# Kernel optimization log

Hardware: AMD Instinct MI355X
Metric: run time of the kernel (lower is better)

The kernel has to match this reference:

```python
import jax, jax.numpy as jnp
import numpy as np

N = 20000      # nodes
E = 320000     # edges (avg degree 16)
D = 256        # embedding_dim
H = 8          # num_heads
DH = D // H    # head_dim = 32
ED = 64        # edge_dim
FF = 4 * D     # feed-forward hidden
EPS = 1e-5


def setup_inputs() -> dict:
    key = jax.random.key(0)
    ks = jax.random.split(key, 32)

    def lin_w(k, i, o):
        return (jax.random.normal(k, (i, o), jnp.float32) / np.sqrt(i)).astype(jnp.float32)

    return {
        "x": jax.random.normal(ks[0], (N, D), jnp.float32),
        "edge_features": jax.random.normal(ks[1], (E, ED), jnp.float32),
        "edge_weights": jax.random.uniform(ks[2], (E,), jnp.float32),
        "edge_index": jax.random.randint(ks[3], (2, E), 0, N, dtype=jnp.int32),
        "Wq": lin_w(ks[4], D, D), "bq": jnp.zeros((D,), jnp.float32),
        "Wk": lin_w(ks[5], D, D), "bk": jnp.zeros((D,), jnp.float32),
        "Wv": lin_w(ks[6], D, D), "bv": jnp.zeros((D,), jnp.float32),
        "We": lin_w(ks[7], ED, DH), "be": jnp.zeros((DH,), jnp.float32),
        "Wo": lin_w(ks[8], D, D), "bo": jnp.zeros((D,), jnp.float32),
        "ln1_g": jnp.ones((D,), jnp.float32), "ln1_b": jnp.zeros((D,), jnp.float32),
        "ln2_g": jnp.ones((D,), jnp.float32), "ln2_b": jnp.zeros((D,), jnp.float32),
        "W1": lin_w(ks[9], D, FF), "b1": jnp.zeros((FF,), jnp.float32),
        "W2": lin_w(ks[10], FF, D), "b2": jnp.zeros((D,), jnp.float32),
        "alpha": jnp.ones((1,), jnp.float32),
        "beta": jnp.ones((1,), jnp.float32),
    }


def _layernorm(x, g, b):
    m = jnp.mean(x, axis=-1, keepdims=True)
    v = jnp.var(x, axis=-1, keepdims=True)
    return (x - m) * jax.lax.rsqrt(v + EPS) * g + b


def _edge_attention(xn, edge_index, ef, ew, Wq, bq, Wk, bk, Wv, bv, We, be, Wo, bo):
    n = xn.shape[0]
    scale = DH ** -0.5
    q = (xn @ Wq + bq).reshape(n, H, DH)
    k = (xn @ Wk + bk).reshape(n, H, DH)
    v = (xn @ Wv + bv).reshape(n, H, DH)
    src, dst = edge_index[0], edge_index[1]
    ep = ef @ We + be                               # [E, DH], shared across heads
    # per-edge, per-head scores: q[dst] . (k[src] + edge_proj)
    scores = jnp.einsum('ehd,ehd->eh', q[dst], k[src] + ep[:, None, :]) * scale
    scores = scores * ew[:, None]
    # segment softmax over incoming edges of each dst node
    m = jax.ops.segment_max(scores, dst, num_segments=n)
    m = jnp.where(jnp.isfinite(m), m, 0.0)          # nodes with no incoming edges
    ex = jnp.exp(scores - m[dst])
    s = jax.ops.segment_sum(ex, dst, num_segments=n)
    attn = ex / s[dst]                              # [E, H]
    # scatter-weighted V aggregation; nodes with no edges stay zero (matches torch)
    out = jax.ops.segment_sum(attn[:, :, None] * v[src], dst, num_segments=n)
    out = out.reshape(n, D) @ Wo + bo
    return out


def reference(x, edge_features, edge_weights, edge_index,
              Wq, bq, Wk, bk, Wv, bv, We, be, Wo, bo,
              ln1_g, ln1_b, ln2_g, ln2_b, W1, b1, W2, b2, alpha, beta):
    xn = _layernorm(x, ln1_g, ln1_b)
    attn_out = _edge_attention(xn, edge_index, edge_features, edge_weights,
                               Wq, bq, Wk, bk, Wv, bv, We, be, Wo, bo)
    x = x + alpha * attn_out
    xn = _layernorm(x, ln2_g, ln2_b)
    ff = jax.nn.gelu(xn @ W1 + b1, approximate=False) @ W2 + b2
    x = x + beta * ff
    return x
```

## Files before the change

kernel.cpp:

```cpp
#include <hip/hip_runtime.h>
#include <math.h>

#define NN 20000
#define EE 320000
#define DD 256
#define HH 8
#define DHD 32
#define EDF 64
#define FFD 1024

typedef unsigned short u16;
typedef __attribute__((ext_vector_type(8))) __bf16 bf16x8;
typedef __attribute__((ext_vector_type(8))) unsigned short u16x8;
typedef __attribute__((ext_vector_type(4))) float f32x4;

#define XN_OFF   (0)
#define AGGB_OFF (2560000)
#define X1_OFF   (5120000)
#define QKV_OFF  (10240000)
#define EP_OFF   (25600000)
#define WT_OFF   (35840000)
#define BQKV_OFF (36240000)
#define CSR_OFF  (36250000)

__device__ __forceinline__ u16 f2bf(float f) {
    unsigned u = __float_as_uint(f);
    return (u16)((u + 0x7FFFu + ((u >> 16) & 1u)) >> 16);
}
__device__ __forceinline__ float bf2f(u16 h) {
    return __uint_as_float(((unsigned)h) << 16);
}
__device__ __forceinline__ float gelu_exact(float v) {
    return 0.5f * v * (1.0f + erff(v * 0.70710678118654752f));
}
__device__ __forceinline__ int xcd_swz(int bid, int nwg) {
    int q = nwg >> 3, r = nwg & 7;
    int xcd = bid & 7, i = bid >> 3;
    return (xcd < r ? xcd * (q + 1) : r * (q + 1) + (xcd - r) * q) + i;
}

#define GLDS16(g, l) __builtin_amdgcn_global_load_lds(             \
    (__attribute__((address_space(1))) void*)(g),                  \
    (__attribute__((address_space(3))) void*)(l), 16, 0, 0)

__device__ __forceinline__ void ln_body(const float* __restrict__ x,
                                        const float* __restrict__ g,
                                        const float* __restrict__ b,
                                        u16* __restrict__ out, int vb) {
    int row = vb * 4 + (threadIdx.x >> 6);
    if (row >= NN) return;
    int lane = threadIdx.x & 63;
    float4 v = *(const float4*)&x[(size_t)row * DD + lane * 4];
    float s  = v.x + v.y + v.z + v.w;
    float ss = v.x * v.x + v.y * v.y + v.z * v.z + v.w * v.w;
    #pragma unroll
    for (int o = 32; o >= 1; o >>= 1) {
        s  += __shfl_xor(s, o);
        ss += __shfl_xor(ss, o);
    }
    float mean = s * (1.0f / DD);
    float var  = ss * (1.0f / DD) - mean * mean;
    float inv  = rsqrtf(var + 1e-5f);
    float4 gg = *(const float4*)&g[lane * 4];
    float4 bb = *(const float4*)&b[lane * 4];
    ushort4 o4;
    o4.x = f2bf((v.x - mean) * inv * gg.x + bb.x);
    o4.y = f2bf((v.y - mean) * inv * gg.y + bb.y);
    o4.z = f2bf((v.z - mean) * inv * gg.z + bb.z);
    o4.w = f2bf((v.w - mean) * inv * gg.w + bb.w);
    *(ushort4*)&out[(size_t)row * DD + lane * 4] = o4;
}

__global__ __launch_bounds__(256) void ln_kernel(const float* __restrict__ x,
                                                 const float* __restrict__ g,
                                                 const float* __restrict__ b,
                                                 u16* __restrict__ out) {
    ln_body(x, g, b, out, blockIdx.x);
}

__device__ __forceinline__ void transp_body(const float* __restrict__ src,
                                            u16* __restrict__ dst,
                                            int K, int N, int k0, int n0) {
    __shared__ float Ws[64][65];
    int t = threadIdx.x;
    int rr = t >> 4, cc = (t & 15) * 4;
    if (n0 + cc < N) {
        #pragma unroll
        for (int p = 0; p < 4; p++) {
            int k = rr + p * 16;
            float4 v = *(const float4*)&src[(size_t)(k0 + k) * N + n0 + cc];
            Ws[k][cc + 0] = v.x; Ws[k][cc + 1] = v.y;
            Ws[k][cc + 2] = v.z; Ws[k][cc + 3] = v.w;
        }
    }
    __syncthreads();
    int n = t >> 2, kc = (t & 3) * 16;
    if (n0 + n < N) {
        u16 o[16];
        #pragma unroll
        for (int j = 0; j < 16; j++) o[j] = f2bf(Ws[kc + j][n]);
        u16* dp = dst + (size_t)(n0 + n) * K + k0 + kc;
        *(ushort4*)(dp + 0)  = *(ushort4*)&o[0];
        *(ushort4*)(dp + 4)  = *(ushort4*)&o[4];
        *(ushort4*)(dp + 8)  = *(ushort4*)&o[8];
        *(ushort4*)(dp + 12) = *(ushort4*)&o[12];
    }
}

__global__ __launch_bounds__(256) void prep_count_ln_kernel(
    const float* __restrict__ Wq, const float* __restrict__ Wk,
    const float* __restrict__ Wv, const float* __restrict__ Wo,
    const float* __restrict__ W1, const float* __restrict__ W2,
    const float* __restrict__ We,
    const float* __restrict__ bq, const float* __restrict__ bk,
    const float* __restrict__ bv,
    u16* __restrict__ WqkvT, u16* __restrict__ WoT, u16* __restrict__ W1T,
    u16* __restrict__ W2T, u16* __restrict__ WeT, float* __restrict__ bqkv,
    const int* __restrict__ ei, int* __restrict__ counts,
    const float* __restrict__ x, const float* __restrict__ ln1g,
    const float* __restrict__ ln1b, u16* __restrict__ xn) {
    int b = blockIdx.x;
    if (b < 193) {
        const float* src; u16* dst; int K, N, ti;
        if      (b < 16)  { src = Wq; dst = WqkvT;          K = 256;  N = 256;  ti = b; }
        else if (b < 32)  { src = Wk; dst = WqkvT + 65536;  K = 256;  N = 256;  ti = b - 16; }
        else if (b < 48)  { src = Wv; dst = WqkvT + 131072; K = 256;  N = 256;  ti = b - 32; }
        else if (b < 64)  { src = Wo; dst = WoT;            K = 256;  N = 256;  ti = b - 48; }
        else if (b < 128) { src = W1; dst = W1T;            K = 256;  N = 1024; ti = b - 64; }
        else if (b < 192) { src = W2; dst = W2T;            K = 1024; N = 256;  ti = b - 128; }
        else              { src = We; dst = WeT;            K = 64;   N = 32;   ti = 0; }
        int ntn = N >> 6; if (ntn == 0) ntn = 1;
        int tk = ti / ntn, tn = ti % ntn;
        transp_body(src, dst, K, N, tk * 64, tn * 64);
    } else if (b == 193) {
        int t = threadIdx.x;
        bqkv[t] = bq[t];
        bqkv[256 + t] = bk[t];
        bqkv[512 + t] = bv[t];
    } else if (b < 1444) {
        int e = (b - 194) * 256 + threadIdx.x;
        if (e < EE) atomicAdd(&counts[ei[EE + e]], 1);
    } else {
        ln_body(x, ln1g, ln1b, xn, b - 1444);
    }
}

template <int BM, int BN, int EPI>
__device__ __forceinline__ void gemm_body(
    char* smem,
    const u16* __restrict__ A, const u16* __restrict__ BT,
    const float* __restrict__ bias,
    float* __restrict__ Cf, u16* __restrict__ Cb,
    const float* __restrict__ res, const float* __restrict__ scale,
    int M, int K, int N, int bxx, int byy)
{
    constexpr int FM = BM / 32, FN = BN / 32;
    constexpr int nA = BM / 32, nB = BN / 32;
    constexpr int NST = (nA > nB) ? nA : nB;
    u16* Asm = (u16*)smem;
    u16* Bsm = (u16*)(smem + BM * 64 * 2);
    const int tid  = threadIdx.x;
    const int lane = tid & 63;
    const int w    = tid >> 6;
    const int wr   = w >> 1, wc = w & 1;
    const int bm   = bxx * BM;
    const int bn   = byy * BN;

    f32x4 acc[FM][FN] = {};

    int st_row[NST], st_src[NST], st_dst[NST];
    #pragma unroll
    for (int i = 0; i < NST; i++) {
        int base  = i * 4096 + w * 1024;
        int off   = base + lane * 16;
        int row   = off >> 7;
        int inner = off & 127;
        st_row[i] = row;
        st_src[i] = (inner ^ ((row & 7) << 4)) >> 1;
        st_dst[i] = base;
    }
    const int arow0 = wr * (BM / 2) + (lane & 15);
    const int brow0 = wc * (BN / 2) + (lane & 15);
    const int kb0   = (lane >> 4) * 16;

    for (int k0 = 0; k0 < K; k0 += 64) {
        #pragma unroll
        for (int i = 0; i < nA; i++) {
            int r = bm + st_row[i]; if (r > M - 1) r = M - 1;
            GLDS16(A + (size_t)r * K + k0 + st_src[i], (char*)Asm + st_dst[i]);
        }
        #pragma unroll
        for (int i = 0; i < nB; i++) {
            int r = bn + st_row[i];
            GLDS16(BT + (size_t)r * K + k0 + st_src[i], (char*)Bsm + st_dst[i]);
        }
        asm volatile("s_waitcnt vmcnt(0)" ::: "memory");
        __syncthreads();
        #pragma unroll
        for (int s = 0; s < 2; s++) {
            bf16x8 af[FM], bfv[FN];
            #pragma unroll
            for (int i = 0; i < FM; i++) {
                int row  = arow0 + i * 16;
                int byte = (row << 7) + ((kb0 + s * 64) ^ ((row & 7) << 4));
                af[i] = *(const bf16x8*)((const char*)Asm + byte);
            }
            #pragma unroll
            for (int j = 0; j < FN; j++) {
                int row  = brow0 + j * 16;
                int byte = (row << 7) + ((kb0 + s * 64) ^ ((row & 7) << 4));
                bfv[j] = *(const bf16x8*)((const char*)Bsm + byte);
            }
            #pragma unroll
            for (int i = 0; i < FM; i++)
                #pragma unroll
                for (int j = 0; j < FN; j++)
                    acc[i][j] = __builtin_amdgcn_mfma_f32_16x16x32_bf16(
                        af[i], bfv[j], acc[i][j], 0, 0, 0);
        }
        __syncthreads();
    }

    float sc = 0.f;
    if constexpr (EPI == 2) sc = scale[0];
    const int col0 = bn + wc * (BN / 2) + (lane & 15);
    const int row0 = bm + wr * (BM / 2) + ((lane >> 4) << 2);
    #pragma unroll
    for (int i = 0; i < FM; i++) {
        #pragma unroll
        for (int j = 0; j < FN; j++) {
            int col = col0 + j * 16;
            float bb = bias[col];
            #pragma unroll
            for (int r = 0; r < 4; r++) {
                int row = row0 + i * 16 + r;
                if (row < M) {
                    float o = acc[i][j][r] + bb;
                    if constexpr (EPI == 1) {
                        Cb[(size_t)row * N + col] = f2bf(gelu_exact(o));
                    } else if constexpr (EPI == 2) {
                        Cf[(size_t)row * N + col] = res[(size_t)row * N + col] + sc * o;
                    } else if constexpr (EPI == 3) {
                        if (col < 256) {
                            Cb[(size_t)row * 256 + col] = f2bf(o * 0.17677669529663689f);
                        } else if (col < 512) {
                            Cb[(size_t)NN * 256 + (size_t)row * 512 + (col - 256)] = f2bf(o);
                        } else {
                            Cb[(size_t)NN * 256 + (size_t)row * 512 + 256 + (col - 512)] = f2bf(o);
                        }
                    } else {
                        Cf[(size_t)row * N + col] = o;
                    }
                }
            }
        }
    }
}

template <int BM, int BN, int EPI>
__global__ __launch_bounds__(256) void gemm_bf16(
    const u16* __restrict__ A, const u16* __restrict__ BT,
    const float* __restrict__ bias,
    float* __restrict__ Cf, u16* __restrict__ Cb,
    const float* __restrict__ res, const float* __restrict__ scale,
    int M, int K, int N, int nwg, int nby) {
    __shared__ char smem[(BM + BN) * 64 * 2];
    int wk = xcd_swz(blockIdx.x, nwg);
    gemm_body<BM, BN, EPI>(smem, A, BT, bias, Cf, Cb, res, scale, M, K, N,
                           wk / nby, wk % nby);
}

__device__ __forceinline__ void ep_body(char* smem,
                                        const float* __restrict__ ef,
                                        const u16* __restrict__ WeT,
                                        const float* __restrict__ be,
                                        const int* __restrict__ epos,
                                        u16* __restrict__ epc, int blk) {
    const int tid  = threadIdx.x;
    const int lane = tid & 63;
    const int w    = tid >> 6;
    const int e0b  = blk * 128;

    #pragma unroll
    for (int j = 0; j < 8; j++) {
        int gidx = (w * 8 + j) * 64 + lane;
        int e    = gidx >> 4;
        int cs   = (gidx & 15) << 4;
        int c    = cs ^ ((e & 15) << 4);
        GLDS16((const char*)ef + (size_t)(e0b + e) * 256 + c,
               smem + (w * 8 + j) * 1024);
    }
    asm volatile("s_waitcnt vmcnt(0)" ::: "memory");
    __syncthreads();

    const int ar = lane & 15;
    f32x4 acc[2][2] = {};
    #pragma unroll
    for (int t = 0; t < 2; t++) {
        int r = w * 32 + t * 16 + ar;
        const char* base = smem + r * 256;
        #pragma unroll
        for (int s = 0; s < 2; s++) {
            int cbyte = (lane >> 4) * 32 + s * 128;
            float4 a0 = *(const float4*)(base + ((cbyte)      ^ (ar << 4)));
            float4 a1 = *(const float4*)(base + ((cbyte + 16) ^ (ar << 4)));
            bf16x8 af;
            af[0] = (__bf16)a0.x; af[1] = (__bf16)a0.y; af[2] = (__bf16)a0.z; af[3] = (__bf16)a0.w;
            af[4] = (__bf16)a1.x; af[5] = (__bf16)a1.y; af[6] = (__bf16)a1.z; af[7] = (__bf16)a1.w;
            #pragma unroll
            for (int j = 0; j < 2; j++) {
                bf16x8 bf = *(const bf16x8*)&WeT[(size_t)(j * 16 + ar) * EDF + s * 32 + ((lane >> 4) * 8)];
                acc[t][j] = __builtin_amdgcn_mfma_f32_16x16x32_bf16(af, bf, acc[t][j], 0, 0, 0);
            }
        }
    }
    __syncthreads();
    u16* outl = (u16*)smem;
    int* posl = (int*)(smem + 8192);
    if (tid < 128) posl[tid] = epos[e0b + tid];
    const int row0 = (lane >> 4) << 2;
    #pragma unroll
    for (int t = 0; t < 2; t++)
        #pragma unroll
        for (int j = 0; j < 2; j++)
            #pragma unroll
            for (int rr = 0; rr < 4; rr++) {
                int row = w * 32 + t * 16 + row0 + rr;
                int col = j * 16 + ar;
                outl[row * 32 + col] = f2bf(acc[t][j][rr] + be[col]);
            }
    __syncthreads();
    #pragma unroll
    for (int c2 = 0; c2 < 2; c2++) {
        int ch = tid + c2 * 256;
        int row = ch >> 2, part = ch & 3;
        u16x8 v = *(const u16x8*)&outl[row * 32 + part * 8];
        *(u16x8*)&epc[(size_t)posl[row] * DHD + part * 8] = v;
    }
}

__global__ __launch_bounds__(256) void qkv_ep_kernel(
    const u16* __restrict__ xn, const u16* __restrict__ WqkvT,
    const float* __restrict__ bqkv, u16* __restrict__ qb,
    const float* __restrict__ ef, const u16* __restrict__ WeT,
    const float* __restrict__ be, const int* __restrict__ epos,
    u16* __restrict__ epc) {
    __shared__ char smem[32768];
    int b = blockIdx.x;
    if (b < 942) {
        int wk = xcd_swz(b, 942);
        gemm_body<128, 128, 3>(smem, xn, WqkvT, bqkv, nullptr, qb, nullptr,
                               nullptr, NN, DD, 768, wk / 6, wk % 6);
    } else {
        ep_body(smem, ef, WeT, be, epos, epc, b - 942);
    }
}

__global__ __launch_bounds__(1024) void scan_kernel(const int* __restrict__ counts,
                                                    int* __restrict__ row_start,
                                                    int* __restrict__ cursor,
                                                    int* __restrict__ dcursor) {
    __shared__ int part[1024];
    __shared__ int hist[64][16];
    const int CH = 20;
    int t = threadIdx.x;
    if (t < 64) {
        #pragma unroll
        for (int s = 0; s < 16; s++) hist[t][s] = 0;
    }
    __syncthreads();
    int base = t * CH;
    int sub = t & 15;
    int loc[CH];
    int s = 0;
    #pragma unroll
    for (int i = 0; i < CH; i++) {
        int idx = base + i;
        int c = (idx < NN) ? counts[idx] : 0;
        if (idx < NN) atomicAdd(&hist[min(c, 63)][sub], 1);
        loc[i] = s;
        s += c;
    }
    part[t] = s;
    __syncthreads();
    for (int o = 1; o < 1024; o <<= 1) {
        int vv = (t >= o) ? part[t - o] : 0;
        __syncthreads();
        part[t] += vv;
        __syncthreads();
    }
    int off = (t > 0) ? part[t - 1] : 0;
    #pragma unroll
    for (int i = 0; i < CH; i++) {
        int idx = base + i;
        if (idx < NN) {
            int rs = off + loc[i];
            row_start[idx] = rs;
            cursor[idx] = rs;
        }
    }
    if (t == 1023) row_start[NN] = part[1023];
    if (t < 64) {
        int st = 0;
        for (int b = 63; b > t; --b) {
            #pragma unroll
            for (int sj = 0; sj < 16; sj++) st += hist[b][sj];
        }
        dcursor[t] = st;
    }
}

__global__ __launch_bounds__(256) void fill_kernel(const int* __restrict__ ei,
                                                   const float* __restrict__ ew,
                                                   int* __restrict__ cursor,
                                                   int2* __restrict__ csr,
                                                   int* __restrict__ epos,
                                                   const int* __restrict__ counts,
                                                   int* __restrict__ dcursor,
                                                   int* __restrict__ order) {
    int b = blockIdx.x;
    if (b < EE / 256) {
        int e = b * 256 + threadIdx.x;
        int src = ei[e];
        int dst = ei[EE + e];
        int pos = atomicAdd(&cursor[dst], 1);
        csr[pos] = make_int2(src, __float_as_int(ew[e] * 1.44269504088896f));
        epos[e] = pos;
    } else {
        __shared__ int lhist[64];
        __shared__ int lbase[64];
        int t = threadIdx.x;
        if (t < 64) lhist[t] = 0;
        __syncthreads();
        int n = (b - EE / 256) * 256 + t;
        int d = -1, lpos = 0;
        if (n < NN) {
            d = min(counts[n], 63);
            lpos = atomicAdd(&lhist[d], 1);
        }
        __syncthreads();
        if (t < 64 && lhist[t] > 0) lbase[t] = atomicAdd(&dcursor[t], lhist[t]);
        __syncthreads();
        if (n < NN) order[lbase[d] + lpos] = n;
    }
}

__global__ __launch_bounds__(256) void attn_kernel(const u16* __restrict__ qb,
                                                   const u16* __restrict__ kv,
                                                   const u16* __restrict__ epc,
                                                   const int2* __restrict__ csr,
                                                   const int* __restrict__ row_start,
                                                   const int* __restrict__ order,
                                                   u16* __restrict__ aggb) {
    const int dst  = order[blockIdx.x * 4 + (threadIdx.x >> 6)];
    const int lane = threadIdx.x & 63;
    const int g    = lane & 7;
    const int d0   = (lane >> 3) * 32 + g * 4;
    const int beg = row_start[dst];
    const int end = row_start[dst + 1];
    ushort4 q4 = *(const ushort4*)&qb[(size_t)dst * DD + d0];
    float4 qv = make_float4(bf2f(q4.x), bf2f(q4.y), bf2f(q4.z), bf2f(q4.w));
    float ss = 0.f;
    float4 acc = make_float4(0.f, 0.f, 0.f, 0.f);

    int i = beg;
    if ((i & 1) && i < end) {
        int2 p = csr[i];
        ushort4 ka = *(const ushort4*)&kv[(size_t)p.x * 512 + d0];
        ushort4 va = *(const ushort4*)&kv[(size_t)p.x * 512 + 256 + d0];
        ushort4 e4 = *(const ushort4*)&epc[(size_t)i * DHD + g * 4];
        float k0 = bf2f(ka.x) + bf2f(e4.x);
        float k1 = bf2f(ka.y) + bf2f(e4.y);
        float k2 = bf2f(ka.z) + bf2f(e4.z);
        float k3 = bf2f(ka.w) + bf2f(e4.w);
        float pv = fmaf(qv.x, k0, fmaf(qv.y, k1, fmaf(qv.z, k2, qv.w * k3)));
        #pragma unroll
        for (int o = 4; o >= 1; o >>= 1) pv += __shfl_xor(pv, o);
        float wq = exp2f(pv * __int_as_float(p.y));
        ss += wq;
        acc.x = fmaf(wq, bf2f(va.x), acc.x);
        acc.y = fmaf(wq, bf2f(va.y), acc.y);
        acc.z = fmaf(wq, bf2f(va.z), acc.z);
        acc.w = fmaf(wq, bf2f(va.w), acc.w);
        ++i;
    }
    for (; i + 4 <= end; i += 4) {
        int4 c01 = *(const int4*)&csr[i];
        int4 c23 = *(const int4*)&csr[i + 2];
        int   sr[4] = {c01.x, c01.z, c23.x, c23.z};
        float wt[4] = {__int_as_float(c01.y), __int_as_float(c01.w),
                       __int_as_float(c23.y), __int_as_float(c23.w)};
        ushort4 ka[4], va[4], e4[4];
        #pragma unroll
        for (int u = 0; u < 4; u++) {
            ka[u] = *(const ushort4*)&kv[(size_t)sr[u] * 512 + d0];
            va[u] = *(const ushort4*)&kv[(size_t)sr[u] * 512 + 256 + d0];
            e4[u] = *(const ushort4*)&epc[(size_t)(i + u) * DHD + g * 4];
        }
        float pp[4];
        #pragma unroll
        for (int u = 0; u < 4; u++) {
            float k0 = bf2f(ka[u].x) + bf2f(e4[u].x);
            float k1 = bf2f(ka[u].y) + bf2f(e4[u].y);
            float k2 = bf2f(ka[u].z) + bf2f(e4[u].z);
            float k3 = bf2f(ka[u].w) + bf2f(e4[u].w);
            pp[u] = fmaf(qv.x, k0, fmaf(qv.y, k1, fmaf(qv.z, k2, qv.w * k3)));
        }
        #pragma unroll
        for (int o = 4; o >= 1; o >>= 1) {
            #pragma unroll
            for (int u = 0; u < 4; u++) pp[u] += __shfl_xor(pp[u], o);
        }
        #pragma unroll
        for (int u = 0; u < 4; u++) {
            float wq = exp2f(pp[u] * wt[u]);
            ss += wq;
            acc.x = fmaf(wq, bf2f(va[u].x), acc.x);
            acc.y = fmaf(wq, bf2f(va[u].y), acc.y);
            acc.z = fmaf(wq, bf2f(va[u].z), acc.z);
            acc.w = fmaf(wq, bf2f(va[u].w), acc.w);
        }
    }
    for (; i < end; ++i) {
        int2 p = csr[i];
        ushort4 ka = *(const ushort4*)&kv[(size_t)p.x * 512 + d0];
        ushort4 va = *(const ushort4*)&kv[(size_t)p.x * 512 + 256 + d0];
        ushort4 e4 = *(const ushort4*)&epc[(size_t)i * DHD + g * 4];
        float k0 = bf2f(ka.x) + bf2f(e4.x);
        float k1 = bf2f(ka.y) + bf2f(e4.y);
        float k2 = bf2f(ka.z) + bf2f(e4.z);
        float k3 = bf2f(ka.w) + bf2f(e4.w);
        float pv = fmaf(qv.x, k0, fmaf(qv.y, k1, fmaf(qv.z, k2, qv.w * k3)));
        #pragma unroll
        for (int o = 4; o >= 1; o >>= 1) pv += __shfl_xor(pv, o);
        float wq = exp2f(pv * __int_as_float(p.y));
        ss += wq;
        acc.x = fmaf(wq, bf2f(va.x), acc.x);
        acc.y = fmaf(wq, bf2f(va.y), acc.y);
        acc.z = fmaf(wq, bf2f(va.z), acc.z);
        acc.w = fmaf(wq, bf2f(va.w), acc.w);
    }
    float inv = (end > beg) ? 1.f / ss : 0.f;
    ushort4 o4;
    o4.x = f2bf(acc.x * inv);
    o4.y = f2bf(acc.y * inv);
    o4.z = f2bf(acc.z * inv);
    o4.w = f2bf(acc.w * inv);
    *(ushort4*)&aggb[(size_t)dst * DD + d0] = o4;
}

extern "C" void kernel_launch(void* const* d_in, const int* in_sizes, int n_in,
                              void* d_out, int out_size, void* d_ws, size_t ws_size,
                              hipStream_t stream) {
    const float* x    = (const float*)d_in[0];
    const float* ef   = (const float*)d_in[1];
    const float* ew   = (const float*)d_in[2];
    const int*   ei   = (const int*)d_in[3];
    const float* Wq   = (const float*)d_in[4];
    const float* bq   = (const float*)d_in[5];
    const float* Wk   = (const float*)d_in[6];
    const float* bk   = (const float*)d_in[7];
    const float* Wv   = (const float*)d_in[8];
    const float* bv   = (const float*)d_in[9];
    const float* We   = (const float*)d_in[10];
    const float* be   = (const float*)d_in[11];
    const float* Wo   = (const float*)d_in[12];
    const float* bo   = (const float*)d_in[13];
    const float* ln1g = (const float*)d_in[14];
    const float* ln1b = (const float*)d_in[15];
    const float* ln2g = (const float*)d_in[16];
    const float* ln2b = (const float*)d_in[17];
    const float* W1   = (const float*)d_in[18];
    const float* b1   = (const float*)d_in[19];
    const float* W2   = (const float*)d_in[20];
    const float* b2   = (const float*)d_in[21];
    const float* alpha = (const float*)d_in[22];
    const float* beta  = (const float*)d_in[23];

    float* ws    = (float*)d_ws;
    u16*   xn    = (u16*)(ws + XN_OFF);
    u16*   aggb  = (u16*)(ws + AGGB_OFF);
    float* x1    = ws + X1_OFF;
    u16*   qb    = (u16*)(ws + QKV_OFF);
    u16*   kv    = qb + (size_t)NN * 256;
    u16*   ff1   = (u16*)(ws + QKV_OFF);
    u16*   epc   = (u16*)(ws + EP_OFF);
    u16*   wt    = (u16*)(ws + WT_OFF);
    u16*   WqkvT = wt;
    u16*   WoT   = wt + 768 * 256;
    u16*   W1T   = WoT + 256 * 256;
    u16*   W2T   = W1T + 1024 * 256;
    u16*   WeT   = W2T + 256 * 1024;
    float* bqkv  = ws + BQKV_OFF;
    float* out   = (float*)d_out;

    int*  counts    = (int*)(ws + CSR_OFF);
    int*  row_start = counts + NN;
    int*  cursor    = row_start + NN + 1;
    int2* csr       = (int2*)(counts + 60004);
    int*  epos      = counts + 60004 + 2 * EE;
    int*  order     = epos + EE;
    int*  dcursor   = order + NN;

    hipMemsetAsync(counts, 0, (size_t)NN * sizeof(int), stream);

    prep_count_ln_kernel<<<6444, 256, 0, stream>>>(
        Wq, Wk, Wv, Wo, W1, W2, We, bq, bk, bv,
        WqkvT, WoT, W1T, W2T, WeT, bqkv, ei, counts, x, ln1g, ln1b, xn);

    scan_kernel<<<1, 1024, 0, stream>>>(counts, row_start, cursor, dcursor);
    fill_kernel<<<EE / 256 + (NN + 255) / 256, 256, 0, stream>>>(
        ei, ew, cursor, csr, epos, counts, dcursor, order);

    qkv_ep_kernel<<<3442, 256, 0, stream>>>(xn, WqkvT, bqkv, qb,
                                            ef, WeT, be, epos, epc);

    attn_kernel<<<NN / 4, 256, 0, stream>>>(qb, kv, epc, csr, row_start, order, aggb);

    gemm_bf16<64, 128, 2><<<626, 256, 0, stream>>>(
        aggb, WoT, bo, x1, nullptr, x, alpha, NN, DD, DD, 626, 2);

    ln_kernel<<<NN / 4, 256, 0, stream>>>(x1, ln2g, ln2b, xn);

    gemm_bf16<128, 128, 1><<<1256, 256, 0, stream>>>(
        xn, W1T, b1, nullptr, ff1, nullptr, nullptr, NN, DD, FFD, 1256, 8);
    gemm_bf16<64, 128, 2><<<626, 256, 0, stream>>>(
        ff1, W2T, b2, out, nullptr, x1, beta, NN, FFD, DD, 626, 2);
}
```

Baseline: 248.6 us.

## Split each destination node's edge list across two wavefronts and combine via LDS

The attention kernel now assigns two wavefronts per destination node, each processing half of the incoming edges, then merges partial softmax sums and weighted V accumulators through shared memory before normalizing and writing. This halves per-wave serial edge-loop latency and doubles the number of waves in flight to hide gather latency. It adds an LDS round-trip, a block-wide barrier, twice the grid size, and duplicate q loads. The odd-index alignment peel still works per half.

```diff
diff --git a/kernel.cpp b/kernel.cpp
--- a/kernel.cpp
+++ b/kernel.cpp
@@ -452,19 +452,24 @@
                                                    const int* __restrict__ row_start,
                                                    const int* __restrict__ order,
                                                    u16* __restrict__ aggb) {
-    const int dst  = order[blockIdx.x * 4 + (threadIdx.x >> 6)];
+    __shared__ float cmb[4][64][6];
+    const int wid  = threadIdx.x >> 6;
+    const int half = wid & 1;
+    const int dst  = order[blockIdx.x * 2 + (wid >> 1)];
     const int lane = threadIdx.x & 63;
     const int g    = lane & 7;
     const int d0   = (lane >> 3) * 32 + g * 4;
     const int beg = row_start[dst];
     const int end = row_start[dst + 1];
+    const int mid = beg + ((end - beg + 1) >> 1);
+    int i  = half ? mid : beg;
+    int eh = half ? end : mid;
     ushort4 q4 = *(const ushort4*)&qb[(size_t)dst * DD + d0];
     float4 qv = make_float4(bf2f(q4.x), bf2f(q4.y), bf2f(q4.z), bf2f(q4.w));
     float ss = 0.f;
     float4 acc = make_float4(0.f, 0.f, 0.f, 0.f);
 
-    int i = beg;
-    if ((i & 1) && i < end) {
+    if ((i & 1) && i < eh) {
         int2 p = csr[i];
         ushort4 ka = *(const ushort4*)&kv[(size_t)p.x * 512 + d0];
         ushort4 va = *(const ushort4*)&kv[(size_t)p.x * 512 + 256 + d0];
@@ -484,7 +489,7 @@
         acc.w = fmaf(wq, bf2f(va.w), acc.w);
         ++i;
     }
-    for (; i + 4 <= end; i += 4) {
+    for (; i + 4 <= eh; i += 4) {
         int4 c01 = *(const int4*)&csr[i];
         int4 c23 = *(const int4*)&csr[i + 2];
         int   sr[4] = {c01.x, c01.z, c23.x, c23.z};
@@ -521,7 +526,7 @@
             acc.w = fmaf(wq, bf2f(va[u].w), acc.w);
         }
     }
-    for (; i < end; ++i) {
+    for (; i < eh; ++i) {
         int2 p = csr[i];
         ushort4 ka = *(const ushort4*)&kv[(size_t)p.x * 512 + d0];
         ushort4 va = *(const ushort4*)&kv[(size_t)p.x * 512 + 256 + d0];
@@ -540,13 +545,26 @@
         acc.z = fmaf(wq, bf2f(va.z), acc.z);
         acc.w = fmaf(wq, bf2f(va.w), acc.w);
     }
-    float inv = (end > beg) ? 1.f / ss : 0.f;
-    ushort4 o4;
-    o4.x = f2bf(acc.x * inv);
-    o4.y = f2bf(acc.y * inv);
-    o4.z = f2bf(acc.z * inv);
-    o4.w = f2bf(acc.w * inv);
-    *(ushort4*)&aggb[(size_t)dst * DD + d0] = o4;
+    cmb[wid][lane][0] = ss;
+    cmb[wid][lane][1] = acc.x;
+    cmb[wid][lane][2] = acc.y;
+    cmb[wid][lane][3] = acc.z;
+    cmb[wid][lane][4] = acc.w;
+    __syncthreads();
+    if (!half) {
+        float sst = ss + cmb[wid + 1][lane][0];
+        float ax = acc.x + cmb[wid + 1][lane][1];
+        float ay = acc.y + cmb[wid + 1][lane][2];
+        float az = acc.z + cmb[wid + 1][lane][3];
+        float aw = acc.w + cmb[wid + 1][lane][4];
+        float inv = (end > beg) ? 1.f / sst : 0.f;
+        ushort4 o4;
+        o4.x = f2bf(ax * inv);
+        o4.y = f2bf(ay * inv);
+        o4.z = f2bf(az * inv);
+        o4.w = f2bf(aw * inv);
+        *(ushort4*)&aggb[(size_t)dst * DD + d0] = o4;
+    }
 }
 
 extern "C" void kernel_launch(void* const* d_in, const int* in_sizes, int n_in,
@@ -615,7 +633,7 @@
     qkv_ep_kernel<<<3442, 256, 0, stream>>>(xn, WqkvT, bqkv, qb,
                                             ef, WeT, be, epos, epc);
 
-    attn_kernel<<<NN / 4, 256, 0, stream>>>(qb, kv, epc, csr, row_start, order, aggb);
+    attn_kernel<<<NN / 2, 256, 0, stream>>>(qb, kv, epc, csr, row_start, order, aggb);
 
     gemm_bf16<64, 128, 2><<<626, 256, 0, stream>>>(
         aggb, WoT, bo, x1, nullptr, x, alpha, NN, DD, DD, 626, 2);
```

After: 250.6 us, median of 2. About the same (+0.8%).

## Fuse second LayerNorm into Wo projection GEMM epilogue with full-row tiles

Applied to the files above, without the earlier changes.

The output-projection GEMM now uses 64x256 tiles, so each block owns complete 256-wide rows. Its epilogue computes the residual add, writes x1, and reduces per-row sums and sums of squares through shuffles and shared memory. It then applies LayerNorm 2 and writes the bf16 normalized activations directly. This removes the separate LN kernel launch and the re-read of x1 from memory. In exchange it halves the grid to 313 blocks and raises epilogue register pressure, and it reads the residual for padded rows past M without a bounds guard.

```diff
diff --git a/kernel.cpp b/kernel.cpp
--- a/kernel.cpp
+++ b/kernel.cpp
@@ -69,13 +69,6 @@
     o4.z = f2bf((v.z - mean) * inv * gg.z + bb.z);
     o4.w = f2bf((v.w - mean) * inv * gg.w + bb.w);
     *(ushort4*)&out[(size_t)row * DD + lane * 4] = o4;
-}
-
-__global__ __launch_bounds__(256) void ln_kernel(const float* __restrict__ x,
-                                                 const float* __restrict__ g,
-                                                 const float* __restrict__ b,
-                                                 u16* __restrict__ out) {
-    ln_body(x, g, b, out, blockIdx.x);
 }
 
 __device__ __forceinline__ void transp_body(const float* __restrict__ src,
@@ -152,7 +145,10 @@
     const float* __restrict__ bias,
     float* __restrict__ Cf, u16* __restrict__ Cb,
     const float* __restrict__ res, const float* __restrict__ scale,
-    int M, int K, int N, int bxx, int byy)
+    int M, int K, int N, int bxx, int byy,
+    const float* __restrict__ lng = nullptr,
+    const float* __restrict__ lnb = nullptr,
+    u16* __restrict__ xnout = nullptr)
 {
     constexpr int FM = BM / 32, FN = BN / 32;
     constexpr int nA = BM / 32, nB = BN / 32;
@@ -221,35 +217,105 @@
         __syncthreads();
     }
 
-    float sc = 0.f;
-    if constexpr (EPI == 2) sc = scale[0];
     const int col0 = bn + wc * (BN / 2) + (lane & 15);
     const int row0 = bm + wr * (BM / 2) + ((lane >> 4) << 2);
-    #pragma unroll
-    for (int i = 0; i < FM; i++) {
-        #pragma unroll
-        for (int j = 0; j < FN; j++) {
-            int col = col0 + j * 16;
-            float bb = bias[col];
+
+    if constexpr (EPI == 4) {
+        float sc = scale[0];
+        float rs[FM][4], rss[FM][4];
+        #pragma unroll
+        for (int i = 0; i < FM; i++)
+            #pragma unroll
+            for (int r = 0; r < 4; r++) { rs[i][r] = 0.f; rss[i][r] = 0.f; }
+        #pragma unroll
+        for (int i = 0; i < FM; i++) {
+            #pragma unroll
+            for (int j = 0; j < FN; j++) {
+                int col = col0 + j * 16;
+                float bb = bias[col];
+                #pragma unroll
+                for (int r = 0; r < 4; r++) {
+                    int row = row0 + i * 16 + r;
+                    float o = res[(size_t)row * N + col] + sc * (acc[i][j][r] + bb);
+                    acc[i][j][r] = o;
+                    if (row < M) Cf[(size_t)row * N + col] = o;
+                    rs[i][r] += o;
+                    rss[i][r] += o * o;
+                }
+            }
+        }
+        #pragma unroll
+        for (int i = 0; i < FM; i++)
             #pragma unroll
             for (int r = 0; r < 4; r++) {
+                #pragma unroll
+                for (int o = 8; o >= 1; o >>= 1) {
+                    rs[i][r]  += __shfl_xor(rs[i][r], o);
+                    rss[i][r] += __shfl_xor(rss[i][r], o);
+                }
+            }
+        float* lnbuf = (float*)smem;
+        if ((lane & 15) == 0) {
+            #pragma unroll
+            for (int i = 0; i < FM; i++)
+                #pragma unroll
+                for (int r = 0; r < 4; r++) {
+                    int lrow = wr * (BM / 2) + ((lane >> 4) << 2) + i * 16 + r;
+                    lnbuf[(lrow * 2 + wc) * 2 + 0] = rs[i][r];
+                    lnbuf[(lrow * 2 + wc) * 2 + 1] = rss[i][r];
+                }
+        }
+        __syncthreads();
+        #pragma unroll
+        for (int i = 0; i < FM; i++) {
+            #pragma unroll
+            for (int r = 0; r < 4; r++) {
+                int lrow = wr * (BM / 2) + ((lane >> 4) << 2) + i * 16 + r;
+                float s2  = lnbuf[(lrow * 2 + 0) * 2 + 0] + lnbuf[(lrow * 2 + 1) * 2 + 0];
+                float ss2 = lnbuf[(lrow * 2 + 0) * 2 + 1] + lnbuf[(lrow * 2 + 1) * 2 + 1];
+                float mean = s2 * (1.0f / DD);
+                float var  = ss2 * (1.0f / DD) - mean * mean;
+                float inv  = rsqrtf(var + 1e-5f);
                 int row = row0 + i * 16 + r;
                 if (row < M) {
-                    float o = acc[i][j][r] + bb;
-                    if constexpr (EPI == 1) {
-                        Cb[(size_t)row * N + col] = f2bf(gelu_exact(o));
-                    } else if constexpr (EPI == 2) {
-                        Cf[(size_t)row * N + col] = res[(size_t)row * N + col] + sc * o;
-                    } else if constexpr (EPI == 3) {
-                        if (col < 256) {
-                            Cb[(size_t)row * 256 + col] = f2bf(o * 0.17677669529663689f);
-                        } else if (col < 512) {
-                            Cb[(size_t)NN * 256 + (size_t)row * 512 + (col - 256)] = f2bf(o);
+                    #pragma unroll
+                    for (int j = 0; j < FN; j++) {
+                        int col = col0 + j * 16;
+                        xnout[(size_t)row * N + col] =
+                            f2bf((acc[i][j][r] - mean) * inv * lng[col] + lnb[col]);
+                    }
+                }
+            }
+        }
+    } else {
+        float sc = 0.f;
+        if constexpr (EPI == 2) sc = scale[0];
+        #pragma unroll
+        for (int i = 0; i < FM; i++) {
+            #pragma unroll
+            for (int j = 0; j < FN; j++) {
+                int col = col0 + j * 16;
+                float bb = bias[col];
+                #pragma unroll
+                for (int r = 0; r < 4; r++) {
+                    int row = row0 + i * 16 + r;
+                    if (row < M) {
+                        float o = acc[i][j][r] + bb;
+                        if constexpr (EPI == 1) {
+                            Cb[(size_t)row * N + col] = f2bf(gelu_exact(o));
+                        } else if constexpr (EPI == 2) {
+                            Cf[(size_t)row * N + col] = res[(size_t)row * N + col] + sc * o;
+                        } else if constexpr (EPI == 3) {
+                            if (col < 256) {
+                                Cb[(size_t)row * 256 + col] = f2bf(o * 0.17677669529663689f);
+                            } else if (col < 512) {
+                                Cb[(size_t)NN * 256 + (size_t)row * 512 + (col - 256)] = f2bf(o);
+                            } else {
+                                Cb[(size_t)NN * 256 + (size_t)row * 512 + 256 + (col - 512)] = f2bf(o);
+                            }
                         } else {
-                            Cb[(size_t)NN * 256 + (size_t)row * 512 + 256 + (col - 512)] = f2bf(o);
+                            Cf[(size_t)row * N + col] = o;
                         }
-                    } else {
-                        Cf[(size_t)row * N + col] = o;
                     }
                 }
             }
@@ -263,11 +329,13 @@
     const float* __restrict__ bias,
     float* __restrict__ Cf, u16* __restrict__ Cb,
     const float* __restrict__ res, const float* __restrict__ scale,
-    int M, int K, int N, int nwg, int nby) {
+    int M, int K, int N, int nwg, int nby,
+    const float* lng = nullptr, const float* lnb = nullptr,
+    u16* xnout = nullptr) {
     __shared__ char smem[(BM + BN) * 64 * 2];
     int wk = xcd_swz(blockIdx.x, nwg);
     gemm_body<BM, BN, EPI>(smem, A, BT, bias, Cf, Cb, res, scale, M, K, N,
-                           wk / nby, wk % nby);
+                           wk / nby, wk % nby, lng, lnb, xnout);
 }
 
 __device__ __forceinline__ void ep_body(char* smem,
@@ -617,10 +685,9 @@
 
     attn_kernel<<<NN / 4, 256, 0, stream>>>(qb, kv, epc, csr, row_start, order, aggb);
 
-    gemm_bf16<64, 128, 2><<<626, 256, 0, stream>>>(
-        aggb, WoT, bo, x1, nullptr, x, alpha, NN, DD, DD, 626, 2);
-
-    ln_kernel<<<NN / 4, 256, 0, stream>>>(x1, ln2g, ln2b, xn);
+    gemm_bf16<64, 256, 4><<<313, 256, 0, stream>>>(
+        aggb, WoT, bo, x1, nullptr, x, alpha, NN, DD, DD, 313, 1,
+        ln2g, ln2b, xn);
 
     gemm_bf16<128, 128, 1><<<1256, 256, 0, stream>>>(
         xn, W1T, b1, nullptr, ff1, nullptr, nullptr, NN, DD, FFD, 1256, 8);
```

Measured after the change: 257.1 us. 1.03x slower.
